# Optimization experiments

Hardware: AMD Instinct MI355X
Metric: run time of the kernel (lower is better)

Reference implementation:

```python
import jax, jax.numpy as jnp
import numpy as np
import math

D_MODEL = 1024
NUM_HEADS = 16
D_K = D_MODEL // NUM_HEADS
MAX_SEQ_LEN = 2048
ROPE_THETA = 10000.0
BATCH = 4
SEQ = 2048


def _rope_buffers():
    inv_freq = 1.0 / (ROPE_THETA ** (jnp.arange(0, D_K, 2, dtype=jnp.float32) / D_K))
    positions = jnp.arange(MAX_SEQ_LEN, dtype=jnp.float32)
    angles = jnp.einsum('i,j->ij', positions, inv_freq)  # [max_seq_len, d_k/2]
    return jnp.cos(angles), jnp.sin(angles)


def setup_inputs() -> dict:
    key = jax.random.key(0)
    kx, kq, kk, kv, ko = jax.random.split(key, 5)
    std = math.sqrt(2.0 / (D_MODEL + D_MODEL))
    x = jax.random.normal(kx, (BATCH, SEQ, D_MODEL), dtype=jnp.float32)
    pos_ids = jnp.broadcast_to(jnp.arange(SEQ, dtype=jnp.int64), (BATCH, SEQ))
    Wq = jax.random.normal(kq, (D_MODEL, D_MODEL), dtype=jnp.float32) * std
    Wk = jax.random.normal(kk, (D_MODEL, D_MODEL), dtype=jnp.float32) * std
    Wv = jax.random.normal(kv, (D_MODEL, D_MODEL), dtype=jnp.float32) * std
    Wo = jax.random.normal(ko, (D_MODEL, D_MODEL), dtype=jnp.float32) * std
    cos, sin = _rope_buffers()
    return {"x": x, "pos_ids": pos_ids, "Wq": Wq, "Wk": Wk, "Wv": Wv, "Wo": Wo, "cos": cos, "sin": sin}


def _apply_rope(t, pos_ids, cos, sin):
    # t: [B, H, S, D_K]; interleaved (even, odd) pair rotation, as in the torch module
    cp = cos[pos_ids][:, None, :, :]  # [B,1,S,D_K/2]
    sp = sin[pos_ids][:, None, :, :]
    tr = t.reshape(*t.shape[:-1], D_K // 2, 2)
    t0, t1 = tr[..., 0], tr[..., 1]
    rot = jnp.stack((t0 * cp - t1 * sp, t0 * sp + t1 * cp), axis=-1)
    return rot.reshape(t.shape)


def reference(x, pos_ids, Wq, Wk, Wv, Wo, cos, sin):
    B, S, _ = x.shape
    def proj(W):
        return jnp.matmul(x, W.T).reshape(B, S, NUM_HEADS, D_K).transpose(0, 2, 1, 3)
    Q = _apply_rope(proj(Wq), pos_ids, cos, sin)
    K = _apply_rope(proj(Wk), pos_ids, cos, sin)
    V = proj(Wv)
    scores = jnp.einsum('bhqd,bhkd->bhqk', Q, K) / math.sqrt(D_K)
    causal = jnp.tril(jnp.ones((S, S), dtype=bool))
    scores = jnp.where(causal, scores, -jnp.inf)
    attn = jax.nn.softmax(scores, axis=-1)
    out = jnp.einsum('bhqk,bhkd->bhqd', attn, V)
    out = out.transpose(0, 2, 1, 3).reshape(B, S, D_MODEL)
    return jnp.matmul(out, Wo.T)
```

## Files before the change

### kernel.cpp

```cpp
#include <hip/hip_runtime.h>
#include <hip/hip_bf16.h>

typedef __bf16 bf16;
typedef __bf16 bf16x4 __attribute__((ext_vector_type(4)));
typedef __bf16 bf16x8 __attribute__((ext_vector_type(8)));
typedef float f32x4 __attribute__((ext_vector_type(4)));
typedef unsigned int u32;

#define BATCH 4
#define SEQN 2048
#define NH 16
#define DK 64
#define DM 1024
#define MROWS (BATCH*SEQN)

__device__ __forceinline__ void async16(bf16* lds, const bf16* g) {
  __builtin_amdgcn_global_load_lds(
      (const __attribute__((address_space(1))) u32*)g,
      (__attribute__((address_space(3))) u32*)lds, 16, 0, 0);
}

__global__ void cvt_all_kernel(const float4* __restrict__ x,  const float4* __restrict__ wq,
                               const float4* __restrict__ wk, const float4* __restrict__ wv,
                               const float4* __restrict__ wo,
                               bf16x4* __restrict__ xb, bf16x4* __restrict__ wqkvb,
                               bf16x4* __restrict__ wob) {
  const int NX = MROWS*DM/4, NW = DM*DM/4;
  int i = blockIdx.x*256 + threadIdx.x;
  const float4* s; bf16x4* d; int j;
  if (i < NX)             { s = x;  d = xb;         j = i; }
  else if (i < NX+NW)     { s = wq; d = wqkvb;      j = i-NX; }
  else if (i < NX+2*NW)   { s = wk; d = wqkvb+NW;   j = i-NX-NW; }
  else if (i < NX+3*NW)   { s = wv; d = wqkvb+2*NW; j = i-NX-2*NW; }
  else if (i < NX+4*NW)   { s = wo; d = wob;        j = i-NX-3*NW; }
  else return;
  float4 f = s[j];
  bf16x4 v;
  v[0] = (bf16)f.x; v[1] = (bf16)f.y; v[2] = (bf16)f.z; v[3] = (bf16)f.w;
  d[j] = v;
}

__device__ __forceinline__ void stage_half(bf16* slot, const bf16* src) {
  const int tid = threadIdx.x; const int w = tid >> 6;
#pragma unroll
  for (int j = 0; j < 2; ++j) {
    int L = j*512 + tid;
    int row = L >> 3;
    int dc  = (L & 7) ^ (row & 7);
    async16(slot + (size_t)(j*512 + w*64)*8, src + (size_t)row*DM + dc*8);
  }
}

#define SBAR() do { __builtin_amdgcn_sched_barrier(0); \
                    __builtin_amdgcn_s_barrier();       \
                    __builtin_amdgcn_sched_barrier(0); } while(0)

#define GPHASE(Ab, Bb, Q, STAGE, FW)  do {                                       \
    bf16x8 afr[2][2];                                                            \
    _Pragma("unroll")                                                            \
    for (int m = 0; m < 2; ++m) {                                                \
      const int row = wm + ((2*(Q)+m)<<4) + lc;                                  \
      _Pragma("unroll")                                                          \
      for (int kk = 0; kk < 2; ++kk)                                             \
        afr[m][kk] = *(const bf16x8*)((Ab) + (size_t)((row<<3) + ((kk*4+quad) ^ (row&7)))*8); \
    }                                                                            \
    if ((Q) == 0) {                                                              \
      _Pragma("unroll")                                                          \
      for (int nt = 0; nt < 4; ++nt) {                                           \
        const int row = wn + (nt<<4) + lc;                                       \
        _Pragma("unroll")                                                        \
        for (int kk = 0; kk < 2; ++kk)                                           \
          bfr[nt][kk] = *(const bf16x8*)((Bb) + (size_t)((row<<3) + ((kk*4+quad) ^ (row&7)))*8); \
      }                                                                          \
    }                                                                            \
    STAGE;                                                                       \
    SBAR();                                                                      \
    asm volatile("s_waitcnt lgkmcnt(0)" ::: "memory");                           \
    __builtin_amdgcn_sched_barrier(0);                                           \
    __builtin_amdgcn_s_setprio(1);                                               \
    _Pragma("unroll")                                                            \
    for (int kk = 0; kk < 2; ++kk)                                               \
      _Pragma("unroll")                                                          \
      for (int m = 0; m < 2; ++m)                                                \
        _Pragma("unroll")                                                        \
        for (int nt = 0; nt < 4; ++nt)                                           \
          acc[2*(Q)+m][nt] = __builtin_amdgcn_mfma_f32_16x16x32_bf16(afr[m][kk], bfr[nt][kk], acc[2*(Q)+m][nt], 0, 0, 0); \
    __builtin_amdgcn_s_setprio(0);                                               \
    FW;                                                                          \
    SBAR();                                                                      \
  } while (0)

__device__ __forceinline__ void gemm_core256(const bf16* __restrict__ Ag,
    const bf16* __restrict__ Bg, int r0, int c0, bf16* sm, f32x4 (&acc)[8][4]) {
  const int tid  = threadIdx.x;
  const int lane = tid & 63, quad = lane >> 4, lc = lane & 15;
  const int w = tid >> 6;
  const int wm = (w >> 2)*128, wn = (w & 3)*64;
  const int NT = DM/64;
  bf16* As[2] = { sm,         sm + 16384 };
  bf16* Bs[2] = { sm + 32768, sm + 49152 };

  auto stA = [&](int t, int h) {
    int tt = t < NT ? t : NT-1;
    stage_half(As[t&1] + h*8192, Ag + (size_t)(r0 + h*128)*DM + tt*64);
  };
  auto stB = [&](int t, int h) {
    int tt = t < NT ? t : NT-1;
    stage_half(Bs[t&1] + h*8192, Bg + (size_t)(c0 + h*128)*DM + tt*64);
  };

  stA(0,0); stA(0,1); stB(0,0); stB(0,1);
  stB(1,0); stB(1,1);
  asm volatile("s_waitcnt vmcnt(4)" ::: "memory");
  SBAR();

  bf16x8 bfr[4][2];
  for (int X = 0; X < NT/2; ++X) {
    const int t0 = 2*X;
    GPHASE(As[0], Bs[0], 0, stA(t0+1,0), );
    GPHASE(As[0], Bs[0], 1, stA(t0+1,1), );
    GPHASE(As[0], Bs[0], 2, stB(t0+2,0), );
    GPHASE(As[0], Bs[0], 3, stB(t0+2,1), asm volatile("s_waitcnt vmcnt(4)" ::: "memory"));
    GPHASE(As[1], Bs[1], 0, stA(t0+2,0), );
    GPHASE(As[1], Bs[1], 1, stA(t0+2,1), );
    GPHASE(As[1], Bs[1], 2, stB(t0+3,0), );
    GPHASE(As[1], Bs[1], 3, stB(t0+3,1), asm volatile("s_waitcnt vmcnt(4)" ::: "memory"));
  }
}

#define BM 128
#define BN 128
__device__ __forceinline__ void gemm_core128(const bf16* __restrict__ A, const bf16* __restrict__ Bt,
                                             int Kdim, int r0, int c0,
                                             bf16* As, bf16* Bs, f32x4 acc[4][4]) {
  const int tid  = threadIdx.x;
  const int wave = tid >> 6, lane = tid & 63;
  const int quad = lane >> 4, lc = lane & 15;
  const int wm = (wave >> 1)*64, wn = (wave & 1)*64;
  for (int k0 = 0; k0 < Kdim; k0 += 64) {
#pragma unroll
    for (int i = 0; i < 4; ++i) {
      int L = i*256 + tid;
      int row = L >> 3;
      int dc  = (L & 7) ^ (row & 7);
      bf16* lbase = As + (size_t)(i*256 + wave*64)*8;
      async16(lbase, A  + (size_t)(r0+row)*Kdim + k0 + dc*8);
      bf16* lbase2 = Bs + (size_t)(i*256 + wave*64)*8;
      async16(lbase2, Bt + (size_t)(c0+row)*Kdim + k0 + dc*8);
    }
    __syncthreads();
#pragma unroll
    for (int kk = 0; kk < 2; ++kk) {
      const int dc = kk*4 + quad;
      bf16x8 af[4], bfr[4];
#pragma unroll
      for (int mt = 0; mt < 4; ++mt) {
        int mr = wm + mt*16 + lc;
        af[mt] = *(const bf16x8*)(As + (size_t)(mr*8 + (dc ^ (mr & 7)))*8);
      }
#pragma unroll
      for (int nt = 0; nt < 4; ++nt) {
        int nr = wn + nt*16 + lc;
        bfr[nt] = *(const bf16x8*)(Bs + (size_t)(nr*8 + (dc ^ (nr & 7)))*8);
      }
#pragma unroll
      for (int mt = 0; mt < 4; ++mt)
#pragma unroll
        for (int nt = 0; nt < 4; ++nt)
          acc[mt][nt] = __builtin_amdgcn_mfma_f32_16x16x32_bf16(af[mt], bfr[nt], acc[mt][nt], 0, 0, 0);
    }
    __syncthreads();
  }
}

#define VS 136
__global__ __launch_bounds__(512, 2) void gemm_qkv_kernel(const bf16* __restrict__ A,
    const bf16* __restrict__ Bt, const float* __restrict__ cosb, const float* __restrict__ sinb,
    bf16* __restrict__ Q, bf16* __restrict__ K, bf16* __restrict__ Vt) {
  __shared__ __align__(16) bf16 sm[65536];
  f32x4 acc[8][4] = {};
  const int r0 = blockIdx.y*256, c0 = blockIdx.x*256;
  gemm_core256(A, Bt, r0, c0, sm, acc);
  const int tid  = threadIdx.x;
  const int lane = tid & 63, quad = lane >> 4, lc = lane & 15;
  const int w = tid >> 6;
  const int wm = (w >> 2)*128, wn = (w & 3)*64;
  const int which = c0 >> 10;
  if (which < 2) {
    bf16* T = which == 0 ? Q : K;
#pragma unroll
    for (int mt = 0; mt < 8; ++mt)
#pragma unroll
      for (int r = 0; r < 4; ++r) {
        int gr = r0 + wm + mt*16 + quad*4 + r;
        int b = gr >> 11, s = gr & (SEQN-1);
#pragma unroll
        for (int nt = 0; nt < 4; ++nt) {
          int gc = c0 + wn + nt*16 + lc;
          int c = gc & (DM-1), h = c >> 6, d = c & 63, p = d >> 1;
          float cc = cosb[s*32 + p], ss = sinb[s*32 + p];
          float v  = acc[mt][nt][r];
          float ov = __shfl_xor(v, 1, 64);
          float outv = ((lc & 1) == 0) ? (v*cc - ov*ss) : (ov*ss + v*cc);
          T[(((size_t)(b*NH + h))*SEQN + s)*DK + d] = (bf16)outv;
        }
      }
  } else {
    asm volatile("s_waitcnt vmcnt(0)" ::: "memory");
    __builtin_amdgcn_sched_barrier(0);
    __syncthreads();
    const int b = r0 >> 11, s_base = r0 & (SEQN-1);
    const int h0 = (c0 & (DM-1)) >> 6;
#pragma unroll
    for (int p = 0; p < 2; ++p) {
      if ((w >> 2) == p) {
#pragma unroll
        for (int mt = 0; mt < 8; ++mt)
#pragma unroll
          for (int nt = 0; nt < 4; ++nt) {
            int col = wn + nt*16 + lc;
            bf16x4 vv;
#pragma unroll
            for (int r = 0; r < 4; ++r) vv[r] = (bf16)acc[mt][nt][r];
            *(bf16x4*)(sm + (size_t)col*VS + mt*16 + quad*4) = vv;
          }
      }
      __syncthreads();
#pragma unroll
      for (int it = 0; it < 8; ++it) {
        int dall = it*32 + (tid >> 4);
        int s_off = (tid & 15)*8;
        bf16x8 vv = *(const bf16x8*)(sm + (size_t)dall*VS + s_off);
        int h = h0 + (dall >> 6), d = dall & 63;
        *(bf16x8*)(Vt + (((size_t)(b*NH + h))*DK + d)*SEQN + s_base + p*128 + s_off) = vv;
      }
      __syncthreads();
    }
  }
}

__global__ __launch_bounds__(256) void gemm_out_kernel(const bf16* __restrict__ A,
    const bf16* __restrict__ Bt, float* __restrict__ C) {
  __shared__ __align__(16) bf16 As[BM*64];
  __shared__ __align__(16) bf16 Bs[BN*64];
  f32x4 acc[4][4] = {};
  const int r0 = blockIdx.y*BM, c0 = blockIdx.x*BN;
  gemm_core128(A, Bt, DM, r0, c0, As, Bs, acc);
  const int tid  = threadIdx.x;
  const int wave = tid >> 6, lane = tid & 63;
  const int quad = lane >> 4, lc = lane & 15;
  const int wm = (wave >> 1)*64, wn = (wave & 1)*64;
#pragma unroll
  for (int mt = 0; mt < 4; ++mt)
#pragma unroll
    for (int nt = 0; nt < 4; ++nt)
#pragma unroll
      for (int r = 0; r < 4; ++r) {
        int gr = r0 + wm + mt*16 + quad*4 + r;
        int gc = c0 + wn + nt*16 + lc;
        C[(size_t)gr*DM + gc] = acc[mt][nt][r];
      }
}

__global__ __launch_bounds__(256, 3) void attn_kernel(const bf16* __restrict__ Q,
    const bf16* __restrict__ K, const bf16* __restrict__ Vt, bf16* __restrict__ Oa) {
  __shared__ __align__(16) bf16 Ks[2][64*64];
  __shared__ __align__(16) bf16 Vs[2][64*64];
  __shared__ __align__(16) bf16 Pw[4][32*72];
  const int tid  = threadIdx.x;
  const int w = tid >> 6, lane = tid & 63;
  const int quad = lane >> 4, lc = lane & 15;
  const int bh = blockIdx.x;
  const int qt = (SEQN/128 - 1) - blockIdx.y;
  const int q0 = qt*128;
  const int qr0 = q0 + w*32;
  const bf16* Qp = Q  + (size_t)bh*SEQN*DK;
  const bf16* Kp = K  + (size_t)bh*SEQN*DK;
  const bf16* Vp = Vt + (size_t)bh*DK*SEQN;
  const float SC = 0.125f * 1.44269504f;
  bf16x8 aq[2][2];
#pragma unroll
  for (int mt = 0; mt < 2; ++mt)
#pragma unroll
    for (int kk = 0; kk < 2; ++kk) {
      bf16x8 raw = *(const bf16x8*)(Qp + (size_t)(qr0 + mt*16 + lc)*DK + kk*32 + quad*8);
#pragma unroll
      for (int j = 0; j < 8; ++j) raw[j] = (bf16)((float)raw[j] * SC);
      aq[mt][kk] = raw;
    }
  f32x4 o[2][4] = {};
  float lrow[2][4] = {};
  bf16* P = Pw[w];
  const int nsteps = 2*(qt + 1);

  auto stage = [&](int kt, int buf) {
#pragma unroll
    for (int j = 0; j < 2; ++j) {
      int L = j*256 + w*64 + lane;
      int row = L >> 3;
      int s8  = (L & 7) ^ (row & 7);
      bf16* kb = &Ks[buf][(size_t)(j*256 + w*64)*8];
      async16(kb, Kp + (size_t)(kt*64 + row)*DK + s8*8);
      bf16* vb = &Vs[buf][(size_t)(j*256 + w*64)*8];
      async16(vb, Vp + (size_t)row*SEQN + kt*64 + s8*8);
    }
  };

  stage(0, 0);
  for (int kt = 0; kt < nsteps; ++kt) {
    const int k0 = kt*64;
    const int cbuf = kt & 1;
    __syncthreads();
    if (kt + 1 < nsteps) stage(kt + 1, cbuf ^ 1);
    if (k0 <= qr0 + 31) {
      const bf16* Kt = Ks[cbuf];
      const bf16* Vc = Vs[cbuf];
      const int lastkey = qr0 + 31;
      f32x4 st[2][4] = {};
#pragma unroll
      for (int kk = 0; kk < 2; ++kk) {
        const int dc = kk*4 + quad;
        bf16x8 bk[4];
#pragma unroll
        for (int nt = 0; nt < 4; ++nt) {
          if (k0 + nt*16 <= lastkey) {
            int kr = nt*16 + lc;
            bk[nt] = *(const bf16x8*)(Kt + (size_t)(kr*8 + (dc ^ (kr & 7)))*8);
          }
        }
#pragma unroll
        for (int nt = 0; nt < 4; ++nt) {
          if (k0 + nt*16 <= lastkey) {
#pragma unroll
            for (int mt = 0; mt < 2; ++mt)
              st[mt][nt] = __builtin_amdgcn_mfma_f32_16x16x32_bf16(aq[mt][kk], bk[nt], st[mt][nt], 0, 0, 0);
          }
        }
      }
#pragma unroll
      for (int mt = 0; mt < 2; ++mt) {
        const int rmin = qr0 + mt*16, rmax = rmin + 15;
#pragma unroll
        for (int nt = 0; nt < 4; ++nt) {
          const int kmin = k0 + nt*16, kmax = kmin + 15;
          f32x4 p;
          if (kmax <= rmin) {
#pragma unroll
            for (int r = 0; r < 4; ++r) p[r] = __builtin_amdgcn_exp2f(st[mt][nt][r]);
          } else if (kmin > rmax) {
            p = f32x4{0.f, 0.f, 0.f, 0.f};
          } else {
            const int key = kmin + lc;
#pragma unroll
            for (int r = 0; r < 4; ++r) {
              float v = __builtin_amdgcn_exp2f(st[mt][nt][r]);
              p[r] = (key > rmin + quad*4 + r) ? 0.f : v;
            }
          }
          st[mt][nt] = p;
#pragma unroll
          for (int r = 0; r < 4; ++r) lrow[mt][r] += p[r];
        }
      }
#pragma unroll
      for (int mt = 0; mt < 2; ++mt)
#pragma unroll
        for (int r = 0; r < 4; ++r)
#pragma unroll
          for (int nt = 0; nt < 4; ++nt)
            P[(mt*16 + quad*4 + r)*72 + nt*16 + lc] = (bf16)st[mt][nt][r];
      asm volatile("s_waitcnt lgkmcnt(0)" ::: "memory");
#pragma unroll
      for (int kk = 0; kk < 2; ++kk) {
        if (k0 + kk*32 <= lastkey) {
          bf16x8 ap[2];
#pragma unroll
          for (int mt = 0; mt < 2; ++mt)
            ap[mt] = *(const bf16x8*)(P + (mt*16 + lc)*72 + kk*32 + quad*8);
          const int kc = kk*4 + quad;
          bf16x8 bv[4];
#pragma unroll
          for (int nb = 0; nb < 4; ++nb) {
            int dr = nb*16 + lc;
            bv[nb] = *(const bf16x8*)(Vc + (size_t)(dr*8 + (kc ^ (dr & 7)))*8);
          }
#pragma unroll
          for (int mt = 0; mt < 2; ++mt)
#pragma unroll
            for (int nb = 0; nb < 4; ++nb)
              o[mt][nb] = __builtin_amdgcn_mfma_f32_16x16x32_bf16(ap[mt], bv[nb], o[mt][nb], 0, 0, 0);
        }
      }
      asm volatile("s_waitcnt lgkmcnt(0)" ::: "memory");
    }
  }
#pragma unroll
  for (int off = 1; off < 16; off <<= 1)
#pragma unroll
    for (int mt = 0; mt < 2; ++mt)
#pragma unroll
      for (int r = 0; r < 4; ++r)
        lrow[mt][r] += __shfl_xor(lrow[mt][r], off, 64);
  const int b = bh >> 4, h = bh & 15;
#pragma unroll
  for (int mt = 0; mt < 2; ++mt)
#pragma unroll
    for (int r = 0; r < 4; ++r) {
      float inv = 1.f / lrow[mt][r];
      int qrow = qr0 + mt*16 + quad*4 + r;
      size_t rowoff = ((size_t)b*SEQN + qrow)*DM + h*DK;
#pragma unroll
      for (int nb = 0; nb < 4; ++nb)
        Oa[rowoff + nb*16 + lc] = (bf16)(o[mt][nb][r]*inv);
    }
}

extern "C" void kernel_launch(void* const* d_in, const int* in_sizes, int n_in,
                              void* d_out, int out_size, void* d_ws, size_t ws_size,
                              hipStream_t stream) {
  const float* x    = (const float*)d_in[0];
  const float* Wq   = (const float*)d_in[2];
  const float* Wk   = (const float*)d_in[3];
  const float* Wv   = (const float*)d_in[4];
  const float* Wo   = (const float*)d_in[5];
  const float* cosb = (const float*)d_in[6];
  const float* sinb = (const float*)d_in[7];
  float* out = (float*)d_out;

  char* ws = (char*)d_ws;
  const size_t SZ_X  = (size_t)MROWS*DM*2;
  const size_t SZ_W  = (size_t)DM*DM*2;
  bf16* xb   = (bf16*)(ws);
  bf16* wqkv = (bf16*)(ws + SZ_X);
  bf16* wo_b = (bf16*)(ws + SZ_X + 3*SZ_W);
  bf16* Qb   = (bf16*)(ws + SZ_X + 4*SZ_W);
  bf16* Kb   = (bf16*)(ws + 2*SZ_X + 4*SZ_W);
  bf16* Vtb  = (bf16*)(ws + 3*SZ_X + 4*SZ_W);
  bf16* Oa   = (bf16*)(ws + 4*SZ_X + 4*SZ_W);

  {
    const int NX = MROWS*DM/4, NW = DM*DM/4;
    int nblk = (NX + 4*NW + 255)/256;
    cvt_all_kernel<<<nblk, 256, 0, stream>>>((const float4*)x, (const float4*)Wq,
        (const float4*)Wk, (const float4*)Wv, (const float4*)Wo,
        (bf16x4*)xb, (bf16x4*)wqkv, (bf16x4*)wo_b);
  }
  gemm_qkv_kernel<<<dim3(3*DM/256, MROWS/256), 512, 0, stream>>>(xb, wqkv, cosb, sinb, Qb, Kb, Vtb);
  attn_kernel<<<dim3(BATCH*NH, SEQN/128), 256, 0, stream>>>(Qb, Kb, Vtb, Oa);
  gemm_out_kernel<<<dim3(DM/BN, MROWS/BM), 256, 0, stream>>>(Oa, wo_b, out);
}
```

Baseline: 256.1 us.

## Shrink QKV GEMM tile to 128x256 with XCD-aware block remap

```diff
diff --git a/kernel.cpp b/kernel.cpp
--- a/kernel.cpp
+++ b/kernel.cpp
@@ -90,42 +90,40 @@
     SBAR();                                                                      \
   } while (0)
 
-__device__ __forceinline__ void gemm_core256(const bf16* __restrict__ Ag,
-    const bf16* __restrict__ Bg, int r0, int c0, bf16* sm, f32x4 (&acc)[8][4]) {
+__device__ __forceinline__ void gemm_core128x256(const bf16* __restrict__ Ag,
+    const bf16* __restrict__ Bg, int r0, int c0, bf16* sm, f32x4 (&acc)[4][4]) {
   const int tid  = threadIdx.x;
   const int lane = tid & 63, quad = lane >> 4, lc = lane & 15;
   const int w = tid >> 6;
-  const int wm = (w >> 2)*128, wn = (w & 3)*64;
+  const int wm = (w >> 2)*64, wn = (w & 3)*64;
   const int NT = DM/64;
-  bf16* As[2] = { sm,         sm + 16384 };
-  bf16* Bs[2] = { sm + 32768, sm + 49152 };
-
-  auto stA = [&](int t, int h) {
-    int tt = t < NT ? t : NT-1;
-    stage_half(As[t&1] + h*8192, Ag + (size_t)(r0 + h*128)*DM + tt*64);
+  bf16* As_[2] = { sm,         sm + 8192  };
+  bf16* Bs_[2] = { sm + 16384, sm + 32768 };
+
+  auto stA = [&](int t) {
+    stage_half(As_[t&1], Ag + (size_t)r0*DM + t*64);
   };
   auto stB = [&](int t, int h) {
-    int tt = t < NT ? t : NT-1;
-    stage_half(Bs[t&1] + h*8192, Bg + (size_t)(c0 + h*128)*DM + tt*64);
+    stage_half(Bs_[t&1] + h*8192, Bg + (size_t)(c0 + h*128)*DM + t*64);
   };
 
-  stA(0,0); stA(0,1); stB(0,0); stB(0,1);
+  stB(0,0); stB(0,1); stA(0);
   stB(1,0); stB(1,1);
   asm volatile("s_waitcnt vmcnt(4)" ::: "memory");
   SBAR();
 
   bf16x8 bfr[4][2];
-  for (int X = 0; X < NT/2; ++X) {
+  for (int X = 0; X < NT/2 - 1; ++X) {
     const int t0 = 2*X;
-    GPHASE(As[0], Bs[0], 0, stA(t0+1,0), );
-    GPHASE(As[0], Bs[0], 1, stA(t0+1,1), );
-    GPHASE(As[0], Bs[0], 2, stB(t0+2,0), );
-    GPHASE(As[0], Bs[0], 3, stB(t0+2,1), asm volatile("s_waitcnt vmcnt(4)" ::: "memory"));
-    GPHASE(As[1], Bs[1], 0, stA(t0+2,0), );
-    GPHASE(As[1], Bs[1], 1, stA(t0+2,1), );
-    GPHASE(As[1], Bs[1], 2, stB(t0+3,0), );
-    GPHASE(As[1], Bs[1], 3, stB(t0+3,1), asm volatile("s_waitcnt vmcnt(4)" ::: "memory"));
-  }
+    GPHASE(As_[0], Bs_[0], 0, stA(t0+1), );
+    GPHASE(As_[0], Bs_[0], 1, stB(t0+2,0); stB(t0+2,1), asm volatile("s_waitcnt vmcnt(4)" ::: "memory"));
+    GPHASE(As_[1], Bs_[1], 0, stA(t0+2), );
+    GPHASE(As_[1], Bs_[1], 1, stB(t0+3,0); stB(t0+3,1), asm volatile("s_waitcnt vmcnt(4)" ::: "memory"));
+  }
+  GPHASE(As_[0], Bs_[0], 0, stA(NT-1), );
+  GPHASE(As_[0], Bs_[0], 1, (void)0, asm volatile("s_waitcnt vmcnt(0)" ::: "memory"));
+  GPHASE(As_[1], Bs_[1], 0, (void)0, );
+  GPHASE(As_[1], Bs_[1], 1, (void)0, );
 }
 
 #define BM 128
@@ -177,19 +175,22 @@
 __global__ __launch_bounds__(512, 2) void gemm_qkv_kernel(const bf16* __restrict__ A,
     const bf16* __restrict__ Bt, const float* __restrict__ cosb, const float* __restrict__ sinb,
     bf16* __restrict__ Q, bf16* __restrict__ K, bf16* __restrict__ Vt) {
-  __shared__ __align__(16) bf16 sm[65536];
-  f32x4 acc[8][4] = {};
-  const int r0 = blockIdx.y*256, c0 = blockIdx.x*256;
-  gemm_core256(A, Bt, r0, c0, sm, acc);
+  __shared__ __align__(16) bf16 sm[49152];
+  f32x4 acc[4][4] = {};
+  const int lin = blockIdx.y * 12 + blockIdx.x;
+  const int xcd = lin & 7, j = lin >> 3;
+  const int by = xcd*8 + (j & 7), bx = j >> 3;
+  const int r0 = by*128, c0 = bx*256;
+  gemm_core128x256(A, Bt, r0, c0, sm, acc);
   const int tid  = threadIdx.x;
   const int lane = tid & 63, quad = lane >> 4, lc = lane & 15;
   const int w = tid >> 6;
-  const int wm = (w >> 2)*128, wn = (w & 3)*64;
+  const int wm = (w >> 2)*64, wn = (w & 3)*64;
   const int which = c0 >> 10;
   if (which < 2) {
     bf16* T = which == 0 ? Q : K;
 #pragma unroll
-    for (int mt = 0; mt < 8; ++mt)
+    for (int mt = 0; mt < 4; ++mt)
 #pragma unroll
       for (int r = 0; r < 4; ++r) {
         int gr = r0 + wm + mt*16 + quad*4 + r;
@@ -209,32 +210,26 @@
     asm volatile("s_waitcnt vmcnt(0)" ::: "memory");
     __builtin_amdgcn_sched_barrier(0);
     __syncthreads();
+#pragma unroll
+    for (int mt = 0; mt < 4; ++mt)
+#pragma unroll
+      for (int nt = 0; nt < 4; ++nt) {
+        int col = wn + nt*16 + lc;
+        bf16x4 vv;
+#pragma unroll
+        for (int r = 0; r < 4; ++r) vv[r] = (bf16)acc[mt][nt][r];
+        *(bf16x4*)(sm + (size_t)col*VS + wm + mt*16 + quad*4) = vv;
+      }
+    __syncthreads();
     const int b = r0 >> 11, s_base = r0 & (SEQN-1);
     const int h0 = (c0 & (DM-1)) >> 6;
 #pragma unroll
-    for (int p = 0; p < 2; ++p) {
-      if ((w >> 2) == p) {
-#pragma unroll
-        for (int mt = 0; mt < 8; ++mt)
-#pragma unroll
-          for (int nt = 0; nt < 4; ++nt) {
-            int col = wn + nt*16 + lc;
-            bf16x4 vv;
-#pragma unroll
-            for (int r = 0; r < 4; ++r) vv[r] = (bf16)acc[mt][nt][r];
-            *(bf16x4*)(sm + (size_t)col*VS + mt*16 + quad*4) = vv;
-          }
-      }
-      __syncthreads();
-#pragma unroll
-      for (int it = 0; it < 8; ++it) {
-        int dall = it*32 + (tid >> 4);
-        int s_off = (tid & 15)*8;
-        bf16x8 vv = *(const bf16x8*)(sm + (size_t)dall*VS + s_off);
-        int h = h0 + (dall >> 6), d = dall & 63;
-        *(bf16x8*)(Vt + (((size_t)(b*NH + h))*DK + d)*SEQN + s_base + p*128 + s_off) = vv;
-      }
-      __syncthreads();
+    for (int it = 0; it < 8; ++it) {
+      int dall = it*32 + (tid >> 4);
+      int s_off = (tid & 15)*8;
+      bf16x8 vv = *(const bf16x8*)(sm + (size_t)dall*VS + s_off);
+      int h = h0 + (dall >> 6), d = dall & 63;
+      *(bf16x8*)(Vt + (((size_t)(b*NH + h))*DK + d)*SEQN + s_base + s_off) = vv;
     }
   }
 }
@@ -445,7 +440,7 @@
         (const float4*)Wk, (const float4*)Wv, (const float4*)Wo,
         (bf16x4*)xb, (bf16x4*)wqkv, (bf16x4*)wo_b);
   }
-  gemm_qkv_kernel<<<dim3(3*DM/256, MROWS/256), 512, 0, stream>>>(xb, wqkv, cosb, sinb, Qb, Kb, Vtb);
+  gemm_qkv_kernel<<<dim3(3*DM/256, MROWS/128), 512, 0, stream>>>(xb, wqkv, cosb, sinb, Qb, Kb, Vtb);
   attn_kernel<<<dim3(BATCH*NH, SEQN/128), 256, 0, stream>>>(Qb, Kb, Vtb, Oa);
   gemm_out_kernel<<<dim3(DM/BN, MROWS/BM), 256, 0, stream>>>(Oa, wo_b, out);
 }
```

After: 262.7 us. +2.6%, slower.
